# Optimization experiments

Hardware: AMD Instinct MI355X
Metric: run time of the kernel (lower is better)

## Reference

```python
import jax, jax.numpy as jnp
import numpy as np

N_BLOCKS = 2
C = 64
N_HEADS = 4
FF = 256
NB_SEQ = 40
SEQ_LEN = 512
NB_PAIRS = (NB_SEQ * (NB_SEQ - 1)) // 2  # 780
B = 2
EPS_ATT = 1e-6


def _ln(x, g, b, eps=1e-5):
    # LayerNorm over last axis (channels)
    mu = jnp.mean(x, axis=-1, keepdims=True)
    var = jnp.var(x, axis=-1, keepdims=True)
    return (x - mu) * jax.lax.rsqrt(var + eps) * g + b


def _kernel_attn(x, wq, bq, wk, bk, wv, bv, wp, bp):
    # x: [B, M, T, C]; faithful to KernelAxialMultiAttention.
    Bs, M, T, Cc = x.shape
    N, D = N_HEADS, Cc // N_HEADS
    q = jax.nn.elu(x @ wq.T + bq) + 1.0
    k = jax.nn.elu(x @ wk.T + bk) + 1.0
    v = x @ wv.T + bv
    q = q.reshape(Bs, M, T, N, D)
    k = k.reshape(Bs, M, T, N, D)
    v = v.reshape(Bs, M, T, N, D)
    ksum = k.sum(axis=2)                                   # [B,M,N,D]
    z = 1.0 / (jnp.einsum('bmtnd,bmnd->bmtn', q, ksum) + EPS_ATT)  # [B,M,T,N]
    ktv = jnp.einsum('bmtnd,bmtne->bmnde', k, v)           # [B,M,N,D,D]
    # Original does Z.expand(...,T,D) @ KtV where Z's D columns are identical,
    # which equals z * column-sum of KtV (sum over first D axis).
    ktv_cs = ktv.sum(axis=-2)                              # [B,M,N,D]
    V = z[..., None] * ktv_cs[:, :, None, :, :]            # [B,M,T,N,D]
    V = V.reshape(Bs, M, T, Cc)
    return V @ wp.T + bp


def setup_inputs() -> dict:
    key = jax.random.key(0)
    ks = iter(jax.random.split(key, 64))

    def w(shape, scale=0.05):
        return jax.random.normal(next(ks), shape, dtype=jnp.float32) * scale

    # seq2pair gather matrix [P, S]
    ii, jj = np.triu_indices(NB_SEQ, 1)
    sp = np.zeros((NB_PAIRS, NB_SEQ), np.float32)
    sp[np.arange(NB_PAIRS), ii] = 1.0
    sp[np.arange(NB_PAIRS), jj] = 1.0

    inp = {
        'x': jax.random.normal(next(ks), (B, 22, SEQ_LEN, NB_SEQ), dtype=jnp.float32),
        'w_in': w((C, 22)), 'b_in': jnp.zeros((C,), jnp.float32),
        'g0': jnp.ones((C,), jnp.float32), 'be0': jnp.zeros((C,), jnp.float32),
        'rqw': w((N_BLOCKS, C, C)), 'rqb': jnp.zeros((N_BLOCKS, C), jnp.float32),
        'rkw': w((N_BLOCKS, C, C)), 'rkb': jnp.zeros((N_BLOCKS, C), jnp.float32),
        'rvw': w((N_BLOCKS, C, C)), 'rvb': jnp.zeros((N_BLOCKS, C), jnp.float32),
        'rpw': w((N_BLOCKS, C, C)), 'rpb': jnp.zeros((N_BLOCKS, C), jnp.float32),
        'cqw': w((N_BLOCKS, C, C)), 'cqb': jnp.zeros((N_BLOCKS, C), jnp.float32),
        'ckw': w((N_BLOCKS, C, C)), 'ckb': jnp.zeros((N_BLOCKS, C), jnp.float32),
        'cvw': w((N_BLOCKS, C, C)), 'cvb': jnp.zeros((N_BLOCKS, C), jnp.float32),
        'cpw': w((N_BLOCKS, C, C)), 'cpb': jnp.zeros((N_BLOCKS, C), jnp.float32),
        'ln_g': jnp.ones((N_BLOCKS, C), jnp.float32), 'ln_b': jnp.zeros((N_BLOCKS, C), jnp.float32),
        'f1w': w((N_BLOCKS, FF, C)), 'f1b': jnp.zeros((N_BLOCKS, FF), jnp.float32),
        'f2w': w((N_BLOCKS, C, FF)), 'f2b': jnp.zeros((N_BLOCKS, C), jnp.float32),
        'wout': w((1, C)), 'bout': jnp.zeros((1,), jnp.float32),
        'seq2pair': jnp.asarray(sp),
    }
    return inp


def reference(x, w_in, b_in, g0, be0, rqw, rqb, rkw, rkb, rvw, rvb, rpw, rpb,
              cqw, cqb, ckw, ckb, cvw, cvb, cpw, cpb, ln_g, ln_b,
              f1w, f1b, f2w, f2b, wout, bout, seq2pair):
    # block_1_1: 1x1 conv (22->64) + ReLU; x: [B,22,L,S] -> h: [B,C,L,S]
    h = jax.nn.relu(jnp.einsum('bcls,dc->bdls', x, w_in) + b_in[None, :, None, None])
    # seq2pair gather-sum: [B,P,L,C] channel-last representation
    hp = jnp.einsum('ps,bdls->bpld', seq2pair, h)
    hp = _ln(hp, g0, be0)
    for i in range(N_BLOCKS):
        # row attention over seq_len axis (M=P, T=L)
        att = _kernel_attn(hp, rqw[i], rqb[i], rkw[i], rkb[i], rvw[i], rvb[i], rpw[i], rpb[i])
        hp = att + hp
        hp = _ln(hp, ln_g[i], ln_b[i])
        # column attention over pairs axis (M=L, T=P)
        hc = jnp.swapaxes(hp, 1, 2)  # [B,L,P,C]
        att = _kernel_attn(hc, cqw[i], cqb[i], ckw[i], ckb[i], cvw[i], cvb[i], cpw[i], cpb[i])
        hp = jnp.swapaxes(att, 1, 2) + hp
        hp = _ln(hp, ln_g[i], ln_b[i])
        # FFN: 1x1 conv 64->256 GELU 256->64, residual
        f = jax.nn.gelu(hp @ f1w[i].T + f1b[i], approximate=False)
        hp = (f @ f2w[i].T + f2b[i]) + hp
        if i != N_BLOCKS - 1:
            hp = _ln(hp, ln_g[i], ln_b[i])
    # pwFNN: 1x1 conv 64->1 + Softplus, then mean over seq_len axis
    y = jax.nn.softplus(hp @ wout.T + bout)[..., 0]   # [B,P,L]
    return jnp.mean(y, axis=-1)                        # [B,P]
```

## Files before the change

### kernel.cpp

```cpp
#include <hip/hip_runtime.h>
#include <math.h>
#include <stdint.h>

#define B_   2
#define S_   40
#define P_   780
#define L_   512
#define C_   64
#define FF_  256
#define NTOK (B_*P_*L_)

typedef __attribute__((ext_vector_type(8))) short short8;
typedef __attribute__((ext_vector_type(4))) float f32x4;
typedef __attribute__((ext_vector_type(4))) unsigned short us4;

__device__ __forceinline__ float ln64(float r, float g, float b) {
    float s1 = r, s2 = r * r;
    #pragma unroll
    for (int m = 1; m < 64; m <<= 1) {
        s1 += __shfl_xor(s1, m, 64);
        s2 += __shfl_xor(s2, m, 64);
    }
    float mu  = s1 * (1.0f / 64.0f);
    float var = s2 * (1.0f / 64.0f) - mu * mu;
    return (r - mu) * rsqrtf(var + 1e-5f) * g + b;
}
__device__ __forceinline__ float gelu_fast(float x) {
    float x2 = x * x;
    float u  = x * fmaf(0.044715f, x2, 1.0f);
    float e  = __builtin_amdgcn_exp2f(u * 2.302265106f);
    return x * e * __builtin_amdgcn_rcpf(e + 1.0f);
}
__device__ __forceinline__ float softplus_f(float v) {
    return (v > 20.0f) ? v : log1pf(__expf(v));
}
__device__ __forceinline__ float elup1(float v) {
    return (v > 0.0f) ? v + 1.0f : __expf(v);
}
__device__ __forceinline__ unsigned short f2bf(float f) {
    union { float f; uint32_t u; } cv; cv.f = f;
    uint32_t u = cv.u;
    return (unsigned short)((u + 0x7FFFu + ((u >> 16) & 1u)) >> 16);
}
__device__ __forceinline__ float bf2f(unsigned short u) {
    union { uint32_t u; float f; } cv; cv.u = (uint32_t)u << 16; return cv.f;
}
__device__ __forceinline__ uint32_t cvtpk(float a, float b) {
    uint32_t d;
    asm("v_cvt_pk_bf16_f32 %0, %1, %2" : "=v"(d) : "v"(a), "v"(b));
    return d;
}

__global__ void k_conv_in(const float* __restrict__ x, const float* __restrict__ w_in,
                          const float* __restrict__ b_in, float* __restrict__ h) {
    int gid = blockIdx.x * 256 + threadIdx.x;
    int c  = gid & 63;
    int tk = gid >> 6;
    if (tk >= B_ * L_ * S_) return;
    int b = tk / (L_ * S_);
    int r = tk % (L_ * S_);
    int l = r / S_;
    int s = r % S_;
    float acc = b_in[c];
    const float* xb = x + (size_t)b * 22 * L_ * S_ + (size_t)l * S_ + s;
    #pragma unroll
    for (int cc = 0; cc < 22; cc++)
        acc = fmaf(xb[(size_t)cc * L_ * S_], w_in[c * 22 + cc], acc);
    h[gid] = fmaxf(acc, 0.0f);
}

__global__ void k_gather_ln(const float* __restrict__ h, const float* __restrict__ g0,
                            const float* __restrict__ be0, unsigned short* __restrict__ hp) {
    int lane = threadIdx.x & 63;
    int wv   = threadIdx.x >> 6;
    int tk = blockIdx.x * 4 + wv;
    if (tk >= NTOK) return;
    int b = tk / (P_ * L_);
    int r = tk % (P_ * L_);
    int p = r / L_;
    int l = r % L_;
    int i = 0, rem = p, cnt = S_ - 1;
    while (rem >= cnt) { rem -= cnt; cnt--; i++; }
    int j = i + 1 + rem;
    const float* hb = h + (((size_t)b * L_ + l) * S_) * 64;
    float v = hb[i * 64 + lane] + hb[j * 64 + lane];
    hp[(size_t)tk * 64 + lane] = f2bf(ln64(v, g0[lane], be0[lane]));
}

__global__ void k_wprep_qkv(const float* __restrict__ rqw, const float* __restrict__ rkw,
                            const float* __restrict__ rvw, const float* __restrict__ cqw,
                            const float* __restrict__ ckw, const float* __restrict__ cvw,
                            unsigned short* __restrict__ qkvf) {
    int g = blockIdx.x * 256 + threadIdx.x;
    if (g >= 6144) return;
    int m = g >> 9, r = g & 511;
    int mat = m >> 1, layer = m & 1;
    int q = r >> 6, lane = r & 63;
    int c = lane & 15, hi = lane >> 4;
    int nt = q >> 1, s = q & 1;
    const float* base;
    switch (mat) {
        case 0: base = rqw; break; case 1: base = rkw; break; case 2: base = rvw; break;
        case 3: base = cqw; break; case 4: base = ckw; break; default: base = cvw; break;
    }
    const float* src = base + layer * 4096 + (nt * 16 + c) * 64 + s * 32 + hi * 8;
    short8 v;
    #pragma unroll
    for (int i = 0; i < 8; i++) v[i] = (short)f2bf(src[i]);
    *(short8*)(qkvf + (size_t)m * 4096 + (size_t)r * 8) = v;
}

__global__ void k_wprep(const float* __restrict__ f1w, const float* __restrict__ f2w,
                        unsigned short* __restrict__ w1s, unsigned short* __restrict__ w2s) {
    int g = blockIdx.x * 256 + threadIdx.x;
    if (g >= 8192) return;
    int layer = g >> 12;
    int rem   = g & 4095;
    int which = rem >> 11;
    int idx   = rem & 2047;
    int l  = idx & 63;
    int q  = idx >> 6;
    int c  = l & 15, hi = l >> 4;
    const float* src;
    unsigned short* dst;
    if (which == 0) {
        int s = q & 1, nt = q >> 1;
        src = f1w + (size_t)layer * 16384 + (nt * 16 + c) * 64 + s * 32 + hi * 8;
        dst = w1s + (size_t)layer * 16384 + (size_t)idx * 8;
    } else {
        int s = q & 7, nt = q >> 3;
        src = f2w + (size_t)layer * 16384 + (nt * 16 + c) * 256 + s * 32 + hi * 8;
        dst = w2s + (size_t)layer * 16384 + (size_t)idx * 8;
    }
    short8 v;
    #pragma unroll
    for (int i = 0; i < 8; i++) v[i] = (short)f2bf(src[i]);
    *(short8*)dst = v;
}

__global__ __launch_bounds__(512) void k_row_fused(
        const unsigned short* __restrict__ hp, unsigned short* __restrict__ hpT,
        const unsigned short* __restrict__ wqf, const unsigned short* __restrict__ wkf,
        const unsigned short* __restrict__ wvf,
        const float* __restrict__ bq, const float* __restrict__ bk,
        const float* __restrict__ bv, const float* __restrict__ wp,
        const float* __restrict__ bp, const float* __restrict__ lng,
        const float* __restrict__ lnb) {
    __shared__ float redK[8][64];
    __shared__ float redV[8][64];
    __shared__ float kvfin[64];
    __shared__ float sksum[64];
    __shared__ float swkv[256];

    const int tid = threadIdx.x, lane = tid & 63, w8 = tid >> 6;
    const int t = lane & 15, hi = lane >> 4;
    const int slice = blockIdx.x;
    const size_t base = (size_t)slice * L_ * 64;

    short8 xkeep[4][2];
    float ks[4][4] = {}, kv[4][4] = {};
    {
        short8 wkfr[4][2], wvfr[4][2];
        #pragma unroll
        for (int nt = 0; nt < 4; nt++)
            #pragma unroll
            for (int s = 0; s < 2; s++) {
                wkfr[nt][s] = *(const short8*)(wkf + ((size_t)((nt*2+s)*64 + lane)) * 8);
                wvfr[nt][s] = *(const short8*)(wvf + ((size_t)((nt*2+s)*64 + lane)) * 8);
            }
        f32x4 bkL[4], bvL[4];
        #pragma unroll
        for (int nt = 0; nt < 4; nt++) {
            bkL[nt] = *(const f32x4*)(bk + nt * 16 + hi * 4);
            bvL[nt] = *(const f32x4*)(bv + nt * 16 + hi * 4);
        }
        #pragma unroll
        for (int it = 0; it < 4; it++) {
            int tok = (w8 + it * 8) * 16 + t;
            const unsigned short* src = hp + base + (size_t)tok * 64;
            #pragma unroll
            for (int s = 0; s < 2; s++)
                xkeep[it][s] = *(const short8*)(src + s * 32 + hi * 8);
            f32x4 aK[4], aV[4];
            #pragma unroll
            for (int nt = 0; nt < 4; nt++) { aK[nt] = (f32x4){0,0,0,0}; aV[nt] = (f32x4){0,0,0,0}; }
            #pragma unroll
            for (int nt = 0; nt < 4; nt++)
                #pragma unroll
                for (int s = 0; s < 2; s++) {
                    aK[nt] = __builtin_amdgcn_mfma_f32_16x16x32_bf16(wkfr[nt][s], xkeep[it][s], aK[nt], 0, 0, 0);
                    aV[nt] = __builtin_amdgcn_mfma_f32_16x16x32_bf16(wvfr[nt][s], xkeep[it][s], aV[nt], 0, 0, 0);
                }
            #pragma unroll
            for (int nt = 0; nt < 4; nt++) {
                float kk[4], vv[4];
                #pragma unroll
                for (int r = 0; r < 4; r++) {
                    kk[r] = elup1(aK[nt][r] + bkL[nt][r]);
                    vv[r] = aV[nt][r] + bvL[nt][r];
                }
                float sp = kk[0] + kk[1] + kk[2] + kk[3];
                sp += __shfl_xor(sp, 16, 64);
                sp += __shfl_xor(sp, 32, 64);
                #pragma unroll
                for (int r = 0; r < 4; r++) { ks[nt][r] += kk[r]; kv[nt][r] += sp * vv[r]; }
            }
        }
    }
    #pragma unroll
    for (int nt = 0; nt < 4; nt++)
        #pragma unroll
        for (int r = 0; r < 4; r++) {
            #pragma unroll
            for (int m = 1; m < 16; m <<= 1) {
                ks[nt][r] += __shfl_xor(ks[nt][r], m, 64);
                kv[nt][r] += __shfl_xor(kv[nt][r], m, 64);
            }
        }
    if (t == 0) {
        #pragma unroll
        for (int nt = 0; nt < 4; nt++)
            #pragma unroll
            for (int r = 0; r < 4; r++) {
                redK[w8][nt * 16 + hi * 4 + r] = ks[nt][r];
                redV[w8][nt * 16 + hi * 4 + r] = kv[nt][r];
            }
    }
    __syncthreads();
    if (tid < 64) {
        float a = 0.0f, b2 = 0.0f;
        #pragma unroll
        for (int w = 0; w < 8; w++) { a += redK[w][tid]; b2 += redV[w][tid]; }
        sksum[tid] = a;
        kvfin[tid] = b2;
    }
    __syncthreads();
    if (tid < 256) {
        int c = tid & 63, n = tid >> 6;
        const float* wpr = wp + c * 64 + n * 16;
        float s = 0.0f;
        #pragma unroll
        for (int e = 0; e < 16; e++) s = fmaf(kvfin[n * 16 + e], wpr[e], s);
        swkv[c * 4 + n] = s;
    }
    __syncthreads();

    short8 wqfr[4][2];
    #pragma unroll
    for (int nt = 0; nt < 4; nt++)
        #pragma unroll
        for (int s = 0; s < 2; s++)
            wqfr[nt][s] = *(const short8*)(wqf + ((size_t)((nt*2+s)*64 + lane)) * 8);
    f32x4 bqL[4], bpL[4], gL[4], bL[4];
    #pragma unroll
    for (int nt = 0; nt < 4; nt++) {
        bqL[nt] = *(const f32x4*)(bq + nt * 16 + hi * 4);
        bpL[nt] = *(const f32x4*)(bp + nt * 16 + hi * 4);
        gL[nt]  = *(const f32x4*)(lng + nt * 16 + hi * 4);
        bL[nt]  = *(const f32x4*)(lnb + nt * 16 + hi * 4);
    }
    const int bb = slice / P_, pp = slice - bb * P_;

    #pragma unroll
    for (int it = 0; it < 4; it++) {
        int tok = (w8 + it * 8) * 16 + t;
        f32x4 aQ[4];
        #pragma unroll
        for (int nt = 0; nt < 4; nt++) aQ[nt] = (f32x4){0,0,0,0};
        #pragma unroll
        for (int nt = 0; nt < 4; nt++)
            #pragma unroll
            for (int s = 0; s < 2; s++)
                aQ[nt] = __builtin_amdgcn_mfma_f32_16x16x32_bf16(wqfr[nt][s], xkeep[it][s], aQ[nt], 0, 0, 0);
        float z[4];
        #pragma unroll
        for (int nt = 0; nt < 4; nt++) {
            f32x4 kS = *(const f32x4*)(sksum + nt * 16 + hi * 4);
            float d = 0.0f;
            #pragma unroll
            for (int r = 0; r < 4; r++)
                d = fmaf(elup1(aQ[nt][r] + bqL[nt][r]), kS[r], d);
            d += __shfl_xor(d, 16, 64);
            d += __shfl_xor(d, 32, 64);
            z[nt] = 1.0f / (d + 1e-6f);
        }
        const unsigned short* srcr = hp + base + (size_t)tok * 64;
        float o[4][4];
        float s1 = 0.0f, s2 = 0.0f;
        #pragma unroll
        for (int nt = 0; nt < 4; nt++) {
            us4 xr4 = *(const us4*)(srcr + nt * 16 + hi * 4);
            #pragma unroll
            for (int r = 0; r < 4; r++) {
                int ch = nt * 16 + hi * 4 + r;
                f32x4 wv4 = *(const f32x4*)(swkv + ch * 4);
                float val = z[0] * wv4[0] + z[1] * wv4[1] + z[2] * wv4[2] + z[3] * wv4[3]
                          + bpL[nt][r] + bf2f(xr4[r]);
                o[nt][r] = val;
                s1 += val; s2 += val * val;
            }
        }
        s1 += __shfl_xor(s1, 16, 64);  s1 += __shfl_xor(s1, 32, 64);
        s2 += __shfl_xor(s2, 16, 64);  s2 += __shfl_xor(s2, 32, 64);
        float mu  = s1 * (1.0f / 64.0f);
        float var = s2 * (1.0f / 64.0f) - mu * mu;
        float rs  = rsqrtf(var + 1e-5f);
        unsigned short* dst = hpT + (((size_t)bb * L_ + tok) * P_ + pp) * 64;
        #pragma unroll
        for (int nt = 0; nt < 4; nt++) {
            float r0 = (o[nt][0] - mu) * rs * gL[nt][0] + bL[nt][0];
            float r1 = (o[nt][1] - mu) * rs * gL[nt][1] + bL[nt][1];
            float r2 = (o[nt][2] - mu) * rs * gL[nt][2] + bL[nt][2];
            float r3 = (o[nt][3] - mu) * rs * gL[nt][3] + bL[nt][3];
            *(uint2*)(dst + nt * 16 + hi * 4) = make_uint2(cvtpk(r0, r1), cvtpk(r2, r3));
        }
    }
}

__global__ __launch_bounds__(512) void k_col_red(
        const unsigned short* __restrict__ xb, const unsigned short* __restrict__ wkf,
        const unsigned short* __restrict__ wvf, const float* __restrict__ bk,
        const float* __restrict__ bv, const float* __restrict__ wp,
        float* __restrict__ stats) {
    __shared__ float redK[8][64];
    __shared__ float redV[8][64];
    __shared__ float kvfin[64];

    const int tid = threadIdx.x, lane = tid & 63, w8 = tid >> 6;
    const int t = lane & 15, hi = lane >> 4;
    const int slice = blockIdx.x;
    const size_t base = (size_t)slice * P_ * 64;

    short8 wkfr[4][2], wvfr[4][2];
    #pragma unroll
    for (int nt = 0; nt < 4; nt++)
        #pragma unroll
        for (int s = 0; s < 2; s++) {
            wkfr[nt][s] = *(const short8*)(wkf + ((size_t)((nt*2+s)*64 + lane)) * 8);
            wvfr[nt][s] = *(const short8*)(wvf + ((size_t)((nt*2+s)*64 + lane)) * 8);
        }
    f32x4 bkL[4], bvL[4];
    #pragma unroll
    for (int nt = 0; nt < 4; nt++) {
        bkL[nt] = *(const f32x4*)(bk + nt * 16 + hi * 4);
        bvL[nt] = *(const f32x4*)(bv + nt * 16 + hi * 4);
    }

    float ks[4][4] = {}, kv[4][4] = {};
    #pragma unroll 1
    for (int tile = w8; tile < 49; tile += 8) {
        int tok = tile * 16 + t;
        bool valid = tok < P_;
        int tokc = valid ? tok : (P_ - 1);
        const unsigned short* src = xb + base + (size_t)tokc * 64;
        short8 xf[2];
        #pragma unroll
        for (int s = 0; s < 2; s++)
            xf[s] = *(const short8*)(src + s * 32 + hi * 8);
        f32x4 aK[4], aV[4];
        #pragma unroll
        for (int nt = 0; nt < 4; nt++) { aK[nt] = (f32x4){0,0,0,0}; aV[nt] = (f32x4){0,0,0,0}; }
        #pragma unroll
        for (int nt = 0; nt < 4; nt++)
            #pragma unroll
            for (int s = 0; s < 2; s++) {
                aK[nt] = __builtin_amdgcn_mfma_f32_16x16x32_bf16(wkfr[nt][s], xf[s], aK[nt], 0, 0, 0);
                aV[nt] = __builtin_amdgcn_mfma_f32_16x16x32_bf16(wvfr[nt][s], xf[s], aV[nt], 0, 0, 0);
            }
        #pragma unroll
        for (int nt = 0; nt < 4; nt++) {
            float kk[4], vv[4];
            #pragma unroll
            for (int r = 0; r < 4; r++) {
                kk[r] = valid ? elup1(aK[nt][r] + bkL[nt][r]) : 0.0f;
                vv[r] = valid ? (aV[nt][r] + bvL[nt][r]) : 0.0f;
            }
            float sp = kk[0] + kk[1] + kk[2] + kk[3];
            sp += __shfl_xor(sp, 16, 64);
            sp += __shfl_xor(sp, 32, 64);
            #pragma unroll
            for (int r = 0; r < 4; r++) { ks[nt][r] += kk[r]; kv[nt][r] += sp * vv[r]; }
        }
    }

    #pragma unroll
    for (int nt = 0; nt < 4; nt++)
        #pragma unroll
        for (int r = 0; r < 4; r++) {
            #pragma unroll
            for (int m = 1; m < 16; m <<= 1) {
                ks[nt][r] += __shfl_xor(ks[nt][r], m, 64);
                kv[nt][r] += __shfl_xor(kv[nt][r], m, 64);
            }
        }
    if (t == 0) {
        #pragma unroll
        for (int nt = 0; nt < 4; nt++)
            #pragma unroll
            for (int r = 0; r < 4; r++) {
                redK[w8][nt * 16 + hi * 4 + r] = ks[nt][r];
                redV[w8][nt * 16 + hi * 4 + r] = kv[nt][r];
            }
    }
    __syncthreads();
    if (tid < 64) {
        float a = 0.0f, b2 = 0.0f;
        #pragma unroll
        for (int w = 0; w < 8; w++) { a += redK[w][tid]; b2 += redV[w][tid]; }
        stats[(size_t)slice * 320 + tid] = a;
        kvfin[tid] = b2;
    }
    __syncthreads();
    if (tid < 256) {
        int c = tid & 63, n = tid >> 6;
        const float* wpr = wp + c * 64 + n * 16;
        float s = 0.0f;
        #pragma unroll
        for (int e = 0; e < 16; e++) s = fmaf(kvfin[n * 16 + e], wpr[e], s);
        stats[(size_t)slice * 320 + 64 + c * 4 + n] = s;
    }
}

template <int MODE>
__global__ __launch_bounds__(256, 2) void k_cmap_ffn2(
        const unsigned short* __restrict__ hpT, unsigned short* __restrict__ hp,
        const unsigned short* __restrict__ wqf,
        const float* __restrict__ bq, const float* __restrict__ bpv,
        const float* __restrict__ stats,
        const unsigned short* __restrict__ w1s, const float* __restrict__ f1b,
        const unsigned short* __restrict__ w2s, const float* __restrict__ f2b,
        const float* __restrict__ lng, const float* __restrict__ lnb,
        const float* __restrict__ wout, const float* __restrict__ bout,
        float* __restrict__ out) {
    __shared__ __align__(16) unsigned char G2[4][2][4096];
    __shared__ float sstat[320];

    const int tid = threadIdx.x, lane = tid & 63, wv = tid >> 6;
    const int t = lane & 15, hi = lane >> 4;
    const int slice = blockIdx.x / 7, tb = blockIdx.x % 7;
    const int bb = slice >> 9, ll = slice & 511;
    const size_t base = (size_t)slice * P_ * 64;

    for (int i = tid; i < 320; i += 256) sstat[i] = stats[(size_t)slice * 320 + i];
    __syncthreads();

    short8 wqfr[4][2];
    #pragma unroll
    for (int nt = 0; nt < 4; nt++)
        #pragma unroll
        for (int s = 0; s < 2; s++)
            wqfr[nt][s] = *(const short8*)(wqf + ((size_t)((nt*2+s)*64 + lane)) * 8);
    f32x4 bqL[4], bpL[4], gL[4], bL[4], f2bL[4];
    #pragma unroll
    for (int nt = 0; nt < 4; nt++) {
        bqL[nt]  = *(const f32x4*)(bq  + nt * 16 + hi * 4);
        bpL[nt]  = *(const f32x4*)(bpv + nt * 16 + hi * 4);
        gL[nt]   = *(const f32x4*)(lng + nt * 16 + hi * 4);
        bL[nt]   = *(const f32x4*)(lnb + nt * 16 + hi * 4);
        f2bL[nt] = *(const f32x4*)(f2b + nt * 16 + hi * 4);
    }

    float vvA[2][4][4];
    short8 xb2A[2][2];
    bool validA[2];
    int pcA[2];

    #pragma unroll
    for (int tt = 0; tt < 2; tt++) {
        int tile = tb * 8 + wv + tt * 4;
        int tilec = (tile < 49) ? tile : 0;
        int p = tilec * 16 + t;
        bool valid = (tile < 49) && (p < P_);
        int pc = (p < P_) ? p : P_ - 1;
        validA[tt] = valid; pcA[tt] = pc;
        const unsigned short* src = hpT + base + (size_t)pc * 64;

        short8 xf[2];
        #pragma unroll
        for (int s = 0; s < 2; s++)
            xf[s] = *(const short8*)(src + s * 32 + hi * 8);
        f32x4 aQ[4];
        #pragma unroll
        for (int nt = 0; nt < 4; nt++) aQ[nt] = (f32x4){0,0,0,0};
        #pragma unroll
        for (int nt = 0; nt < 4; nt++)
            #pragma unroll
            for (int s = 0; s < 2; s++)
                aQ[nt] = __builtin_amdgcn_mfma_f32_16x16x32_bf16(wqfr[nt][s], xf[s], aQ[nt], 0, 0, 0);
        float z[4];
        #pragma unroll
        for (int nt = 0; nt < 4; nt++) {
            f32x4 kS = *(const f32x4*)(sstat + nt * 16 + hi * 4);
            float d = 0.0f;
            #pragma unroll
            for (int r = 0; r < 4; r++)
                d = fmaf(elup1(aQ[nt][r] + bqL[nt][r]), kS[r], d);
            d += __shfl_xor(d, 16, 64);
            d += __shfl_xor(d, 32, 64);
            z[nt] = 1.0f / (d + 1e-6f);
        }
        float s1 = 0.0f, s2 = 0.0f;
        #pragma unroll
        for (int nt = 0; nt < 4; nt++) {
            us4 xr4 = *(const us4*)(src + nt * 16 + hi * 4);
            #pragma unroll
            for (int r = 0; r < 4; r++) {
                int ch = nt * 16 + hi * 4 + r;
                f32x4 wv4 = *(const f32x4*)(sstat + 64 + ch * 4);
                float val = z[0] * wv4[0] + z[1] * wv4[1] + z[2] * wv4[2] + z[3] * wv4[3]
                          + bpL[nt][r] + bf2f(xr4[r]);
                vvA[tt][nt][r] = val;
                s1 += val; s2 += val * val;
            }
        }
        s1 += __shfl_xor(s1, 16, 64);  s1 += __shfl_xor(s1, 32, 64);
        s2 += __shfl_xor(s2, 16, 64);  s2 += __shfl_xor(s2, 32, 64);
        float mu  = s1 * (1.0f / 64.0f);
        float var = s2 * (1.0f / 64.0f) - mu * mu;
        float rs  = rsqrtf(var + 1e-5f);
        #pragma unroll
        for (int nt = 0; nt < 4; nt++)
            #pragma unroll
            for (int r = 0; r < 4; r++)
                vvA[tt][nt][r] = (vvA[tt][nt][r] - mu) * rs * gL[nt][r] + bL[nt][r];

        unsigned char* yw = &G2[wv][tt][0];
        #pragma unroll
        for (int nt = 0; nt < 4; nt++) {
            uint2 w = make_uint2(cvtpk(vvA[tt][nt][0], vvA[tt][nt][1]),
                                 cvtpk(vvA[tt][nt][2], vvA[tt][nt][3]));
            uint32_t ch0 = nt * 16 + hi * 4;
            uint32_t boff = (uint32_t)t * 128 + ((ch0 >> 3) ^ (uint32_t)(t & 7)) * 16 + (ch0 & 7) * 2;
            *(uint2*)(yw + boff) = w;
        }
        #pragma unroll
        for (int s = 0; s < 2; s++)
            xb2A[tt][s] = *(short8*)(yw + (uint32_t)t * 128 +
                                     (((uint32_t)(s * 4 + hi)) ^ (uint32_t)(t & 7)) * 16);
    }

    f32x4 acc2A[2][4];
    #pragma unroll
    for (int tt = 0; tt < 2; tt++)
        #pragma unroll
        for (int n2 = 0; n2 < 4; n2++) acc2A[tt][n2] = f2bL[n2];

    #pragma unroll
    for (int half = 0; half < 2; half++) {
        #pragma unroll
        for (int ntl = 0; ntl < 8; ntl++) {
            int nt = half * 8 + ntl;
            f32x4 b1 = *(const f32x4*)(f1b + nt * 16 + hi * 4);
            f32x4 accA[2] = { b1, b1 };
            #pragma unroll
            for (int s = 0; s < 2; s++) {
                short8 wf = *(const short8*)(w1s + ((size_t)(nt * 2 + s) * 64 + lane) * 8);
                accA[0] = __builtin_amdgcn_mfma_f32_16x16x32_bf16(wf, xb2A[0][s], accA[0], 0, 0, 0);
                accA[1] = __builtin_amdgcn_mfma_f32_16x16x32_bf16(wf, xb2A[1][s], accA[1], 0, 0, 0);
            }
            uint32_t woff = ((uint32_t)(ntl * 32 + hi * 8)) ^ ((uint32_t)(t & 7) << 4);
            #pragma unroll
            for (int tt = 0; tt < 2; tt++) {
                uint32_t p0 = cvtpk(gelu_fast(accA[tt][0]), gelu_fast(accA[tt][1]));
                uint32_t p1 = cvtpk(gelu_fast(accA[tt][2]), gelu_fast(accA[tt][3]));
                *(uint2*)(&G2[wv][tt][0] + t * 256 + woff) = make_uint2(p0, p1);
            }
        }
        #pragma unroll
        for (int sl = 0; sl < 4; sl++) {
            int s = half * 4 + sl;
            uint32_t roff = ((uint32_t)(sl * 64 + hi * 16)) ^ ((uint32_t)(t & 7) << 4);
            short8 faA[2];
            #pragma unroll
            for (int tt = 0; tt < 2; tt++)
                faA[tt] = *(short8*)(&G2[wv][tt][0] + t * 256 + roff);
            #pragma unroll
            for (int n2 = 0; n2 < 4; n2++) {
                short8 wf = *(const short8*)(w2s + ((size_t)(n2 * 8 + s) * 64 + lane) * 8);
                acc2A[0][n2] = __builtin_amdgcn_mfma_f32_16x16x32_bf16(wf, faA[0], acc2A[0][n2], 0, 0, 0);
                acc2A[1][n2] = __builtin_amdgcn_mfma_f32_16x16x32_bf16(wf, faA[1], acc2A[1][n2], 0, 0, 0);
            }
        }
    }

    #pragma unroll
    for (int tt = 0; tt < 2; tt++) {
        float vo[4][4];
        float s1 = 0.0f, s2 = 0.0f;
        #pragma unroll
        for (int n2 = 0; n2 < 4; n2++)
            #pragma unroll
            for (int r = 0; r < 4; r++) {
                float v = acc2A[tt][n2][r] + vvA[tt][n2][r];
                vo[n2][r] = v;
                s1 += v; s2 += v * v;
            }
        if (MODE == 0) {
            s1 += __shfl_xor(s1, 16, 64);  s1 += __shfl_xor(s1, 32, 64);
            s2 += __shfl_xor(s2, 16, 64);  s2 += __shfl_xor(s2, 32, 64);
            float mu  = s1 * (1.0f / 64.0f);
            float var = s2 * (1.0f / 64.0f) - mu * mu;
            float rs  = rsqrtf(var + 1e-5f);
            if (validA[tt]) {
                unsigned short* dst = hp + (((size_t)bb * P_ + pcA[tt]) * L_ + ll) * 64;
                #pragma unroll
                for (int n2 = 0; n2 < 4; n2++) {
                    float r0 = (vo[n2][0] - mu) * rs * gL[n2][0] + bL[n2][0];
                    float r1 = (vo[n2][1] - mu) * rs * gL[n2][1] + bL[n2][1];
                    float r2 = (vo[n2][2] - mu) * rs * gL[n2][2] + bL[n2][2];
                    float r3 = (vo[n2][3] - mu) * rs * gL[n2][3] + bL[n2][3];
                    *(uint2*)(dst + n2 * 16 + hi * 4) = make_uint2(cvtpk(r0, r1), cvtpk(r2, r3));
                }
            }
        } else {
            float part = 0.0f;
            #pragma unroll
            for (int n2 = 0; n2 < 4; n2++) {
                f32x4 w4 = *(const f32x4*)(wout + n2 * 16 + hi * 4);
                #pragma unroll
                for (int r = 0; r < 4; r++)
                    part = fmaf(vo[n2][r], w4[r], part);
            }
            part += __shfl_xor(part, 16, 64);
            part += __shfl_xor(part, 32, 64);
            if (hi == 0 && validA[tt]) {
                float sp = softplus_f(part + bout[0]);
                atomicAdd(out + bb * P_ + pcA[tt], sp * (1.0f / L_));
            }
        }
    }
}

extern "C" void kernel_launch(void* const* d_in, const int* in_sizes, int n_in,
                              void* d_out, int out_size, void* d_ws, size_t ws_size,
                              hipStream_t stream) {
    const float* x    = (const float*)d_in[0];
    const float* w_in = (const float*)d_in[1];
    const float* b_in = (const float*)d_in[2];
    const float* g0   = (const float*)d_in[3];
    const float* be0  = (const float*)d_in[4];
    const float* rqw  = (const float*)d_in[5];  const float* rqb = (const float*)d_in[6];
    const float* rkw  = (const float*)d_in[7];  const float* rkb = (const float*)d_in[8];
    const float* rvw  = (const float*)d_in[9];  const float* rvb = (const float*)d_in[10];
    const float* rpw  = (const float*)d_in[11]; const float* rpb = (const float*)d_in[12];
    const float* cqw  = (const float*)d_in[13]; const float* cqb = (const float*)d_in[14];
    const float* ckw  = (const float*)d_in[15]; const float* ckb = (const float*)d_in[16];
    const float* cvw  = (const float*)d_in[17]; const float* cvb = (const float*)d_in[18];
    const float* cpw  = (const float*)d_in[19]; const float* cpb = (const float*)d_in[20];
    const float* lng  = (const float*)d_in[21]; const float* lnb = (const float*)d_in[22];
    const float* f1w  = (const float*)d_in[23]; const float* f1b = (const float*)d_in[24];
    const float* f2w  = (const float*)d_in[25]; const float* f2b = (const float*)d_in[26];
    const float* wout = (const float*)d_in[27]; const float* bout= (const float*)d_in[28];
    float* out = (float*)d_out;

    unsigned short* hp  = (unsigned short*)d_ws;
    unsigned short* hpT = hp + (size_t)NTOK * 64;
    float* h = (float*)(hpT + (size_t)NTOK * 64);
    unsigned short* w1s  = (unsigned short*)h;
    unsigned short* w2s  = w1s + 2 * 16384;
    unsigned short* qkvf = w2s + 2 * 16384;
    float* stats = (float*)(qkvf + 12 * 4096);

    hipMemsetAsync(out, 0, (size_t)out_size * sizeof(float), stream);

    k_conv_in<<<(B_ * L_ * S_ * 64) / 256, 256, 0, stream>>>(x, w_in, b_in, h);
    k_gather_ln<<<NTOK / 4, 256, 0, stream>>>(h, g0, be0, hp);
    k_wprep<<<32, 256, 0, stream>>>(f1w, f2w, w1s, w2s);
    k_wprep_qkv<<<24, 256, 0, stream>>>(rqw, rkw, rvw, cqw, ckw, cvw, qkvf);

    for (int i = 0; i < 2; i++) {
        k_row_fused<<<B_ * P_, 512, 0, stream>>>(hp, hpT,
            qkvf + (size_t)(0 + i) * 4096, qkvf + (size_t)(2 + i) * 4096,
            qkvf + (size_t)(4 + i) * 4096,
            rqb + i * 64, rkb + i * 64, rvb + i * 64, rpw + i * 4096, rpb + i * 64,
            lng + i * 64, lnb + i * 64);
        k_col_red<<<B_ * L_, 512, 0, stream>>>(hpT,
            qkvf + (size_t)(8 + i) * 4096, qkvf + (size_t)(10 + i) * 4096,
            ckb + i * 64, cvb + i * 64, cpw + i * 4096, stats);
        if (i == 0) {
            k_cmap_ffn2<0><<<B_ * L_ * 7, 256, 0, stream>>>(hpT, hp,
                qkvf + (size_t)(6 + i) * 4096, cqb + i * 64, cpb + i * 64, stats,
                w1s + (size_t)i * 16384, f1b + i * 256,
                w2s + (size_t)i * 16384, f2b + i * 64,
                lng + i * 64, lnb + i * 64, wout, bout, out);
        } else {
            k_cmap_ffn2<1><<<B_ * L_ * 7, 256, 0, stream>>>(hpT, hp,
                qkvf + (size_t)(6 + i) * 4096, cqb + i * 64, cpb + i * 64, stats,
                w1s + (size_t)i * 16384, f1b + i * 256,
                w2s + (size_t)i * 16384, f2b + i * 64,
                lng + i * 64, lnb + i * 64, wout, bout, out);
        }
    }
}
```

Before: 1.017 ms.

## Process three pair-tiles per wave in column-map FFN kernel, pack residual as bf16

Each wave in the fused column-attention-output + FFN kernel now handles three 16-token tiles instead of two. The grid drops from 7 to 5 blocks per slice, so each FFN weight fragment loaded from global memory feeds more MFMAs. The post-LayerNorm residual is now kept in registers as packed bf16 words rather than fp32 to offset the extra register pressure. Waves with no valid tile exit early. The costs are a larger LDS staging buffer, more padded tile slots per slice, and the residual added after the FFN is now rounded to bf16.

```diff
diff --git a/kernel.cpp b/kernel.cpp
--- a/kernel.cpp
+++ b/kernel.cpp
@@ -44,6 +44,12 @@
 }
 __device__ __forceinline__ float bf2f(unsigned short u) {
     union { uint32_t u; float f; } cv; cv.u = (uint32_t)u << 16; return cv.f;
+}
+__device__ __forceinline__ float bflo(uint32_t w) {
+    union { uint32_t u; float f; } cv; cv.u = w << 16; return cv.f;
+}
+__device__ __forceinline__ float bfhi(uint32_t w) {
+    union { uint32_t u; float f; } cv; cv.u = w & 0xffff0000u; return cv.f;
 }
 __device__ __forceinline__ uint32_t cvtpk(float a, float b) {
     uint32_t d;
@@ -422,7 +428,7 @@
 }
 
 template <int MODE>
-__global__ __launch_bounds__(256, 2) void k_cmap_ffn2(
+__global__ __launch_bounds__(256, 2) void k_cmap_ffn3(
         const unsigned short* __restrict__ hpT, unsigned short* __restrict__ hp,
         const unsigned short* __restrict__ wqf,
         const float* __restrict__ bq, const float* __restrict__ bpv,
@@ -432,17 +438,18 @@
         const float* __restrict__ lng, const float* __restrict__ lnb,
         const float* __restrict__ wout, const float* __restrict__ bout,
         float* __restrict__ out) {
-    __shared__ __align__(16) unsigned char G2[4][2][4096];
+    __shared__ __align__(16) unsigned char G2[4][3][4096];
     __shared__ float sstat[320];
 
     const int tid = threadIdx.x, lane = tid & 63, wv = tid >> 6;
     const int t = lane & 15, hi = lane >> 4;
-    const int slice = blockIdx.x / 7, tb = blockIdx.x % 7;
+    const int slice = blockIdx.x / 5, tb = blockIdx.x % 5;
     const int bb = slice >> 9, ll = slice & 511;
     const size_t base = (size_t)slice * P_ * 64;
 
     for (int i = tid; i < 320; i += 256) sstat[i] = stats[(size_t)slice * 320 + i];
     __syncthreads();
+    if (tb * 12 + wv >= 49) return;
 
     short8 wqfr[4][2];
     #pragma unroll
@@ -460,17 +467,17 @@
         f2bL[nt] = *(const f32x4*)(f2b + nt * 16 + hi * 4);
     }
 
-    float vvA[2][4][4];
-    short8 xb2A[2][2];
-    bool validA[2];
-    int pcA[2];
-
-    #pragma unroll
-    for (int tt = 0; tt < 2; tt++) {
-        int tile = tb * 8 + wv + tt * 4;
-        int tilec = (tile < 49) ? tile : 0;
-        int p = tilec * 16 + t;
-        bool valid = (tile < 49) && (p < P_);
+    uint32_t pw[3][8];
+    short8 xb2A[3][2];
+    bool validA[3];
+    int pcA[3];
+
+    #pragma unroll
+    for (int tt = 0; tt < 3; tt++) {
+        int slot = tb * 12 + tt * 4 + wv;
+        int slotc = (slot < 49) ? slot : 48;
+        int p = slotc * 16 + t;
+        bool valid = (slot < 49) && (p < P_);
         int pc = (p < P_) ? p : P_ - 1;
         validA[tt] = valid; pcA[tt] = pc;
         const unsigned short* src = hpT + base + (size_t)pc * 64;
@@ -499,6 +506,7 @@
             d += __shfl_xor(d, 32, 64);
             z[nt] = 1.0f / (d + 1e-6f);
         }
+        float vv[4][4];
         float s1 = 0.0f, s2 = 0.0f;
         #pragma unroll
         for (int nt = 0; nt < 4; nt++) {
@@ -509,7 +517,7 @@
                 f32x4 wv4 = *(const f32x4*)(sstat + 64 + ch * 4);
                 float val = z[0] * wv4[0] + z[1] * wv4[1] + z[2] * wv4[2] + z[3] * wv4[3]
                           + bpL[nt][r] + bf2f(xr4[r]);
-                vvA[tt][nt][r] = val;
+                vv[nt][r] = val;
                 s1 += val; s2 += val * val;
             }
         }
@@ -519,19 +527,21 @@
         float var = s2 * (1.0f / 64.0f) - mu * mu;
         float rs  = rsqrtf(var + 1e-5f);
         #pragma unroll
-        for (int nt = 0; nt < 4; nt++)
-            #pragma unroll
-            for (int r = 0; r < 4; r++)
-                vvA[tt][nt][r] = (vvA[tt][nt][r] - mu) * rs * gL[nt][r] + bL[nt][r];
+        for (int nt = 0; nt < 4; nt++) {
+            float r0 = (vv[nt][0] - mu) * rs * gL[nt][0] + bL[nt][0];
+            float r1 = (vv[nt][1] - mu) * rs * gL[nt][1] + bL[nt][1];
+            float r2 = (vv[nt][2] - mu) * rs * gL[nt][2] + bL[nt][2];
+            float r3 = (vv[nt][3] - mu) * rs * gL[nt][3] + bL[nt][3];
+            pw[tt][nt * 2]     = cvtpk(r0, r1);
+            pw[tt][nt * 2 + 1] = cvtpk(r2, r3);
+        }
 
         unsigned char* yw = &G2[wv][tt][0];
         #pragma unroll
         for (int nt = 0; nt < 4; nt++) {
-            uint2 w = make_uint2(cvtpk(vvA[tt][nt][0], vvA[tt][nt][1]),
-                                 cvtpk(vvA[tt][nt][2], vvA[tt][nt][3]));
             uint32_t ch0 = nt * 16 + hi * 4;
             uint32_t boff = (uint32_t)t * 128 + ((ch0 >> 3) ^ (uint32_t)(t & 7)) * 16 + (ch0 & 7) * 2;
-            *(uint2*)(yw + boff) = w;
+            *(uint2*)(yw + boff) = make_uint2(pw[tt][nt * 2], pw[tt][nt * 2 + 1]);
         }
         #pragma unroll
         for (int s = 0; s < 2; s++)
@@ -539,9 +549,9 @@
                                      (((uint32_t)(s * 4 + hi)) ^ (uint32_t)(t & 7)) * 16);
     }
 
-    f32x4 acc2A[2][4];
-    #pragma unroll
-    for (int tt = 0; tt < 2; tt++)
+    f32x4 acc2A[3][4];
+    #pragma unroll
+    for (int tt = 0; tt < 3; tt++)
         #pragma unroll
         for (int n2 = 0; n2 < 4; n2++) acc2A[tt][n2] = f2bL[n2];
 
@@ -551,16 +561,17 @@
         for (int ntl = 0; ntl < 8; ntl++) {
             int nt = half * 8 + ntl;
             f32x4 b1 = *(const f32x4*)(f1b + nt * 16 + hi * 4);
-            f32x4 accA[2] = { b1, b1 };
+            f32x4 accA[3] = { b1, b1, b1 };
             #pragma unroll
             for (int s = 0; s < 2; s++) {
                 short8 wf = *(const short8*)(w1s + ((size_t)(nt * 2 + s) * 64 + lane) * 8);
                 accA[0] = __builtin_amdgcn_mfma_f32_16x16x32_bf16(wf, xb2A[0][s], accA[0], 0, 0, 0);
                 accA[1] = __builtin_amdgcn_mfma_f32_16x16x32_bf16(wf, xb2A[1][s], accA[1], 0, 0, 0);
+                accA[2] = __builtin_amdgcn_mfma_f32_16x16x32_bf16(wf, xb2A[2][s], accA[2], 0, 0, 0);
             }
             uint32_t woff = ((uint32_t)(ntl * 32 + hi * 8)) ^ ((uint32_t)(t & 7) << 4);
             #pragma unroll
-            for (int tt = 0; tt < 2; tt++) {
+            for (int tt = 0; tt < 3; tt++) {
                 uint32_t p0 = cvtpk(gelu_fast(accA[tt][0]), gelu_fast(accA[tt][1]));
                 uint32_t p1 = cvtpk(gelu_fast(accA[tt][2]), gelu_fast(accA[tt][3]));
                 *(uint2*)(&G2[wv][tt][0] + t * 256 + woff) = make_uint2(p0, p1);
@@ -570,31 +581,37 @@
         for (int sl = 0; sl < 4; sl++) {
             int s = half * 4 + sl;
             uint32_t roff = ((uint32_t)(sl * 64 + hi * 16)) ^ ((uint32_t)(t & 7) << 4);
-            short8 faA[2];
-            #pragma unroll
-            for (int tt = 0; tt < 2; tt++)
+            short8 faA[3];
+            #pragma unroll
+            for (int tt = 0; tt < 3; tt++)
                 faA[tt] = *(short8*)(&G2[wv][tt][0] + t * 256 + roff);
             #pragma unroll
             for (int n2 = 0; n2 < 4; n2++) {
                 short8 wf = *(const short8*)(w2s + ((size_t)(n2 * 8 + s) * 64 + lane) * 8);
                 acc2A[0][n2] = __builtin_amdgcn_mfma_f32_16x16x32_bf16(wf, faA[0], acc2A[0][n2], 0, 0, 0);
                 acc2A[1][n2] = __builtin_amdgcn_mfma_f32_16x16x32_bf16(wf, faA[1], acc2A[1][n2], 0, 0, 0);
-            }
-        }
-    }
-
-    #pragma unroll
-    for (int tt = 0; tt < 2; tt++) {
+                acc2A[2][n2] = __builtin_amdgcn_mfma_f32_16x16x32_bf16(wf, faA[2], acc2A[2][n2], 0, 0, 0);
+            }
+        }
+    }
+
+    #pragma unroll
+    for (int tt = 0; tt < 3; tt++) {
         float vo[4][4];
         float s1 = 0.0f, s2 = 0.0f;
         #pragma unroll
-        for (int n2 = 0; n2 < 4; n2++)
-            #pragma unroll
-            for (int r = 0; r < 4; r++) {
-                float v = acc2A[tt][n2][r] + vvA[tt][n2][r];
-                vo[n2][r] = v;
-                s1 += v; s2 += v * v;
-            }
+        for (int n2 = 0; n2 < 4; n2++) {
+            float y0 = bflo(pw[tt][n2 * 2]);
+            float y1 = bfhi(pw[tt][n2 * 2]);
+            float y2 = bflo(pw[tt][n2 * 2 + 1]);
+            float y3 = bfhi(pw[tt][n2 * 2 + 1]);
+            vo[n2][0] = acc2A[tt][n2][0] + y0;
+            vo[n2][1] = acc2A[tt][n2][1] + y1;
+            vo[n2][2] = acc2A[tt][n2][2] + y2;
+            vo[n2][3] = acc2A[tt][n2][3] + y3;
+            #pragma unroll
+            for (int r = 0; r < 4; r++) { s1 += vo[n2][r]; s2 += vo[n2][r] * vo[n2][r]; }
+        }
         if (MODE == 0) {
             s1 += __shfl_xor(s1, 16, 64);  s1 += __shfl_xor(s1, 32, 64);
             s2 += __shfl_xor(s2, 16, 64);  s2 += __shfl_xor(s2, 32, 64);
@@ -678,13 +695,13 @@
             qkvf + (size_t)(8 + i) * 4096, qkvf + (size_t)(10 + i) * 4096,
             ckb + i * 64, cvb + i * 64, cpw + i * 4096, stats);
         if (i == 0) {
-            k_cmap_ffn2<0><<<B_ * L_ * 7, 256, 0, stream>>>(hpT, hp,
+            k_cmap_ffn3<0><<<B_ * L_ * 5, 256, 0, stream>>>(hpT, hp,
                 qkvf + (size_t)(6 + i) * 4096, cqb + i * 64, cpb + i * 64, stats,
                 w1s + (size_t)i * 16384, f1b + i * 256,
                 w2s + (size_t)i * 16384, f2b + i * 64,
                 lng + i * 64, lnb + i * 64, wout, bout, out);
         } else {
-            k_cmap_ffn2<1><<<B_ * L_ * 7, 256, 0, stream>>>(hpT, hp,
+            k_cmap_ffn3<1><<<B_ * L_ * 5, 256, 0, stream>>>(hpT, hp,
                 qkvf + (size_t)(6 + i) * 4096, cqb + i * 64, cpb + i * 64, stats,
                 w1s + (size_t)i * 16384, f1b + i * 256,
                 w2s + (size_t)i * 16384, f2b + i * 64,
```

Measured after the change: 941.0 us, median of 3. 1.08x faster.
